# Performance work log

Hardware: AMD Instinct MI355X
Metric: run time of the kernel (lower is better)

Reference implementation:

```python
import jax, jax.numpy as jnp
import numpy as np

PIXEL_W = 1.0
EPS = 1e-8
BIG = 1e10


def extract_zero_crossings(s):
    """Vectorized marching-squares-style zero-crossing extraction.
    s: (H, W) SDF. Returns padded points (N, 2) float and validity mask (N,) bool,
    N = (H-1)*W + H*(W-1), in the same (vertical pairs first, then horizontal)
    order as the original python loops."""
    H, W = s.shape
    dt = s.dtype
    # vertical neighbor pairs (i, j) vs (i+1, j)
    v1, v2 = s[:-1, :], s[1:, :]
    ii = jnp.broadcast_to(jnp.arange(H - 1, dtype=dt)[:, None], (H - 1, W))
    jj = jnp.broadcast_to(jnp.arange(W, dtype=dt)[None, :], (H - 1, W))
    c1 = v1 == 0
    c2 = (~c1) & (v2 == 0)
    cx = (~c1) & (~c2) & (v1 * v2 < 0)
    alpha = jnp.abs(v1) / (jnp.abs(v1) + jnp.abs(v2) + EPS)
    row = jnp.where(c1, ii, jnp.where(c2, ii + 1.0, ii + alpha))
    pts_v = jnp.stack([row, jj], axis=-1).reshape(-1, 2)
    m_v = (c1 | c2 | cx).reshape(-1)
    # horizontal neighbor pairs (i, j) vs (i, j+1)
    h1, h2 = s[:, :-1], s[:, 1:]
    ii2 = jnp.broadcast_to(jnp.arange(H, dtype=dt)[:, None], (H, W - 1))
    jj2 = jnp.broadcast_to(jnp.arange(W - 1, dtype=dt)[None, :], (H, W - 1))
    d1 = h1 == 0
    d2 = (~d1) & (h2 == 0)
    dx = (~d1) & (~d2) & (h1 * h2 < 0)
    beta = jnp.abs(h1) / (jnp.abs(h1) + jnp.abs(h2) + EPS)
    col = jnp.where(d1, jj2, jnp.where(d2, jj2 + 1.0, jj2 + beta))
    pts_h = jnp.stack([ii2, col], axis=-1).reshape(-1, 2)
    m_h = (d1 | d2 | dx).reshape(-1)
    return jnp.concatenate([pts_v, pts_h], 0), jnp.concatenate([m_v, m_h], 0)


def pairwise_dist(p, g):
    # (Np, Ng) euclidean distances via the gram trick (avoids (Np,Ng,2) temp)
    d2 = jnp.sum(p * p, 1)[:, None] + jnp.sum(g * g, 1)[None, :] - 2.0 * (p @ g.T)
    return jnp.sqrt(jnp.maximum(d2, 0.0))


def masked_chamfer(pp, pm, gp, gm):
    # chamfer as in compute_chamfer_distance: -mean(min over gt) + mean(min over pred)
    d = pairwise_dist(pp, gp)
    d = jnp.where(pm[:, None] & gm[None, :], d, BIG)
    min_p = jnp.min(d, axis=1)
    min_g = jnp.min(d, axis=0)
    np_ = jnp.maximum(jnp.sum(pm), 1)
    ng_ = jnp.maximum(jnp.sum(gm), 1)
    return -jnp.sum(jnp.where(pm, min_p, 0.0)) / np_ + jnp.sum(jnp.where(gm, min_g, 0.0)) / ng_


def setup_inputs() -> dict:
    key = jax.random.key(0)
    k1, k2 = jax.random.split(key)
    B, H, W = 2, 80, 80
    return {
        "pred_logits": jax.random.normal(k1, (B, 1, H, W), dtype=jnp.float32),
        "gt_sdf": jax.random.normal(k2, (B, 1, H, W), dtype=jnp.float32),
    }


def reference(pred_logits, gt_sdf):
    pred = pred_logits[:, 0]  # (B, H, W)
    gt = gt_sdf[:, 0]
    pixel_loss = jnp.mean(jnp.abs(pred - gt))
    chamfers = []
    for b in range(pred.shape[0]):  # small fixed batch loop
        pp, pm = extract_zero_crossings(pred[b])
        gp, gm = extract_zero_crossings(gt[b])
        chamfers.append(masked_chamfer(pp, pm, gp, gm))
    loss = PIXEL_W * pixel_loss
    last_chamfer = jnp.mean(jnp.stack(chamfers))
    return loss, last_chamfer
```

## Files before the change

### kernel.cpp

```cpp
#include <hip/hip_runtime.h>

#define HH 80
#define WW 80
#define IMG (HH * WW)
#define NV ((HH - 1) * WW)
#define NPTS (NV + HH * (WW - 1))
#define NPIX (2 * IMG)
#define BIGF 1.0e10f
#define INVC 1.0e7f
#define EPSF 1e-8f
#define QSCALE 131072.0f

#define SETPAD 12800
#define SBLOCKS (SETPAD / 256)
#define EXBLOCKS (4 * SBLOCKS)
#define PXBLOCKS (NPIX / 256)
#define PREPB (EXBLOCKS + PXBLOCKS)

#define BLK 256
#define APT 8
#define ACHUNK (BLK * APT)
#define ABLOCKS ((NPTS + ACHUNK - 1) / ACHUNK)
#define NSLICE 64
#define MAXSLICE ((((NPTS + NSLICE - 1) / NSLICE) + 1) & ~1)
#define MAXP2 (MAXSLICE / 2)

#define CNT_STRIDE 32
#define PIX_OFF 512
#define TICKET_OFF 640
#define SUM_OFF 768
#define SCALAR_BYTES 1024

typedef float f32x2 __attribute__((ext_vector_type(2)));

__device__ __forceinline__ long long wave_reduce_ll(long long v) {
#pragma unroll
  for (int o = 32; o > 0; o >>= 1) {
    int2 p = *(int2*)&v;
    p.x = __shfl_down(p.x, o, 64);
    p.y = __shfl_down(p.y, o, 64);
    v += *(long long*)&p;
  }
  return v;
}

__global__ void k_zero(unsigned int* __restrict__ w) {
  w[threadIdx.x] = 0u;
}

__global__ void __launch_bounds__(256) k_prep(
    const float* __restrict__ pred, const float* __restrict__ gt,
    float2* __restrict__ pts, float* __restrict__ minarr,
    int* __restrict__ cnt, unsigned long long* __restrict__ pix_i) {
  __shared__ int wc[4], wo[4];
  __shared__ long long rl[4];
  int tid = threadIdx.x, lane = tid & 63, wid = tid >> 6;
  int gtid = blockIdx.x * 256 + tid;

  if (gtid < 4 * NPTS) minarr[gtid] = BIGF;

  if (blockIdx.x < EXBLOCKS) {
    int set = blockIdx.x / SBLOCKS;
    int idx = (blockIdx.x % SBLOCKS) * 256 + tid;
    const float* s = (set < 2 ? pred : gt) + (set & 1) * IMG;
    float r = 0.f, c = 0.f;
    bool valid = false;
    if (idx < NPTS) {
      if (idx < NV) {
        int i = idx / WW, j = idx - i * WW;
        float v1 = s[i * WW + j], v2 = s[(i + 1) * WW + j];
        c = (float)j;
        if (v1 == 0.f)      { r = (float)i;       valid = true; }
        else if (v2 == 0.f) { r = (float)i + 1.f; valid = true; }
        else {
          r = (float)i + fabsf(v1) / (fabsf(v1) + fabsf(v2) + EPSF);
          valid = (v1 * v2 < 0.f);
        }
      } else {
        int t = idx - NV;
        int i = t / (WW - 1), j = t - i * (WW - 1);
        float h1 = s[i * WW + j], h2 = s[i * WW + j + 1];
        r = (float)i;
        if (h1 == 0.f)      { c = (float)j;       valid = true; }
        else if (h2 == 0.f) { c = (float)j + 1.f; valid = true; }
        else {
          c = (float)j + fabsf(h1) / (fabsf(h1) + fabsf(h2) + EPSF);
          valid = (h1 * h2 < 0.f);
        }
      }
    }
    unsigned long long mask = __ballot(valid);
    int nw = __popcll(mask);
    if (lane == 0) wc[wid] = nw;
    __syncthreads();
    if (tid == 0) {
      int t0 = wc[0], t1 = wc[1], t2 = wc[2], t3 = wc[3];
      int tot = t0 + t1 + t2 + t3;
      int base = tot ? atomicAdd(&cnt[set * CNT_STRIDE], tot) : 0;
      wo[0] = base; wo[1] = base + t0; wo[2] = base + t0 + t1;
      wo[3] = base + t0 + t1 + t2;
    }
    __syncthreads();
    if (valid) {
      int lpos = __popcll(mask & ((1ull << lane) - 1ull));
      pts[set * NPTS + wo[wid] + lpos] = make_float2(r, c);
    }
  } else {
    int p = (blockIdx.x - EXBLOCKS) * 256 + tid;
    float d = fabsf(pred[p] - gt[p]);
    long long q = (long long)(d * QSCALE + 0.5f);
    q = wave_reduce_ll(q);
    if (lane == 0) rl[wid] = q;
    __syncthreads();
    if (tid == 0)
      atomicAdd(pix_i, (unsigned long long)(rl[0] + rl[1] + rl[2] + rl[3]));
  }
}

__global__ void __launch_bounds__(BLK) k_min(
    const float2* __restrict__ pts, float* __restrict__ minarr,
    const int* __restrict__ cnt) {
  int dir = blockIdx.z;
  int Aset = ((dir & 1) << 1) | (dir >> 1);
  int Bset = Aset ^ 2;
  int cntA = cnt[Aset * CNT_STRIDE], cntB = cnt[Bset * CNT_STRIDE];

  int abase0 = blockIdx.x * ACHUNK;
  if (abase0 >= cntA) return;
  int slicelen = (((cntB + NSLICE - 1) / NSLICE) + 1) & ~1;
  int b0 = blockIdx.y * slicelen;
  if (b0 >= cntB) return;
  int n = min(slicelen, cntB - b0);
  int sn = (n + 1) & ~1;

  __shared__ f32x2 qx_s[MAXP2], qy_s[MAXP2], q2_s[MAXP2];
  for (int i = threadIdx.x; i < sn; i += BLK) {
    float2 q = (i < n) ? pts[Bset * NPTS + b0 + i] : make_float2(INVC, INVC);
    ((float*)qx_s)[i] = q.x;
    ((float*)qy_s)[i] = q.y;
    ((float*)q2_s)[i] = fmaf(q.x, q.x, q.y * q.y);
  }
  __syncthreads();

  int abase = abase0 + threadIdx.x;
  f32x2 nxv[APT], nyv[APT];
  float p2v[APT], m[APT];
#pragma unroll
  for (int i = 0; i < APT; ++i) {
    int a = abase + i * BLK;
    float2 p = (a < cntA) ? pts[Aset * NPTS + a] : make_float2(0.f, 0.f);
    float nx = -2.f * p.x, ny = -2.f * p.y;
    nxv[i].x = nx; nxv[i].y = nx;
    nyv[i].x = ny; nyv[i].y = ny;
    p2v[i] = fmaf(p.x, p.x, p.y * p.y);
    m[i] = 3.0e38f;
  }

  int np2 = sn >> 1;
#pragma unroll 2
  for (int p = 0; p < np2; ++p) {
    f32x2 qx = qx_s[p], qy = qy_s[p], q2 = q2_s[p];
#pragma unroll
    for (int i = 0; i < APT; ++i) {
      f32x2 u = __builtin_elementwise_fma(
          nyv[i], qy, __builtin_elementwise_fma(nxv[i], qx, q2));
      m[i] = fminf(fminf(u.x, u.y), m[i]);
    }
  }

#pragma unroll
  for (int i = 0; i < APT; ++i) {
    int a = abase + i * BLK;
    if (a < cntA) {
      float d2 = fmaxf(m[i] + p2v[i], 0.f);
      unsigned int mine = __float_as_uint(d2);
      unsigned int* addr = (unsigned int*)&minarr[Aset * NPTS + a];
      unsigned int cur = __hip_atomic_load(addr, __ATOMIC_RELAXED,
                                           __HIP_MEMORY_SCOPE_AGENT);
      if (mine < cur) atomicMin(addr, mine);
    }
  }
}

__global__ void __launch_bounds__(256) k_fin(
    const float* __restrict__ minarr, const int* __restrict__ cnt,
    const unsigned long long* __restrict__ pix_i,
    unsigned long long* __restrict__ sum_i,
    unsigned int* __restrict__ ticket, float* __restrict__ out) {
  int set = blockIdx.x >> 2, q = blockIdx.x & 3;
  int tid = threadIdx.x, lane = tid & 63;
  int n = cnt[set * CNT_STRIDE];

  long long ls = 0;
  for (int i = q * 256 + tid; i < n; i += 1024) {
    float d = sqrtf(minarr[set * NPTS + i]);
    ls += (long long)(d * QSCALE + 0.5f);
  }
  ls = wave_reduce_ll(ls);
  if (lane == 0) atomicAdd(&sum_i[set], (unsigned long long)ls);
  __syncthreads();

  if (tid == 0) {
    __threadfence();
    unsigned int t = atomicAdd(ticket, 1u);
    if (t == 15u) {
      const float iq = 1.0f / QSCALE;
      float ss[4];
      for (int k = 0; k < 4; ++k)
        ss[k] = (float)((long long)atomicAdd(&sum_i[k], 0ull)) * iq;
      float n0 = fmaxf((float)cnt[0 * CNT_STRIDE], 1.f);
      float n1 = fmaxf((float)cnt[1 * CNT_STRIDE], 1.f);
      float n2 = fmaxf((float)cnt[2 * CNT_STRIDE], 1.f);
      float n3 = fmaxf((float)cnt[3 * CNT_STRIDE], 1.f);
      float ch0 = -ss[0] / n0 + ss[2] / n2;
      float ch1 = -ss[1] / n1 + ss[3] / n3;
      out[0] = (float)(long long)(*pix_i) * iq / (float)NPIX;
      out[1] = 0.5f * (ch0 + ch1);
    }
  }
}

extern "C" void kernel_launch(void* const* d_in, const int* in_sizes, int n_in,
                              void* d_out, int out_size, void* d_ws, size_t ws_size,
                              hipStream_t stream) {
  const float* pred = (const float*)d_in[0];
  const float* gt   = (const float*)d_in[1];
  float* out = (float*)d_out;

  int* cnt = (int*)d_ws;
  unsigned long long* pix_i = (unsigned long long*)((char*)d_ws + PIX_OFF);
  unsigned int* ticket = (unsigned int*)((char*)d_ws + TICKET_OFF);
  unsigned long long* sum_i = (unsigned long long*)((char*)d_ws + SUM_OFF);
  float2* pts   = (float2*)((char*)d_ws + SCALAR_BYTES);
  float* minarr = (float*)((char*)d_ws + SCALAR_BYTES + sizeof(float2) * 4 * NPTS);

  k_zero<<<1, 256, 0, stream>>>((unsigned int*)d_ws);
  k_prep<<<PREPB, 256, 0, stream>>>(pred, gt, pts, minarr, cnt, pix_i);
  k_min<<<dim3(ABLOCKS, NSLICE, 4), BLK, 0, stream>>>(pts, minarr, cnt);
  k_fin<<<16, 256, 0, stream>>>(minarr, cnt, pix_i, sum_i, ticket, out);
}
```

Baseline: 38.75 us.

## Replace global atomic compaction with per-segment counts and drop zeroing kernel

Zero-crossing points are now compacted per 256-wide segment with per-segment counts, not through a global atomic counter, so the separate zero-init kernel can be removed. The pixel loss goes into per-block partial sums that the final kernel reduces. The min kernel tiles over segment groups (8 A-segments by 2 B-segments), picks 4 or 8 points per thread from the count, and maps thread indices to segments with prefix offsets. This saves one launch and the atomic contention, at the cost of more index arithmetic and a fixed grid that may contain many empty or lightly loaded blocks.

Measured after the change: 43.57 us. 12.4% more time.

```diff
diff --git a/kernel.cpp b/kernel.cpp
--- a/kernel.cpp
+++ b/kernel.cpp
@@ -11,25 +11,18 @@
 #define EPSF 1e-8f
 #define QSCALE 131072.0f
 
-#define SETPAD 12800
-#define SBLOCKS (SETPAD / 256)
-#define EXBLOCKS (4 * SBLOCKS)
-#define PXBLOCKS (NPIX / 256)
+#define NSEG 50
+#define SEGPAD 64
+#define SETSLOTS (NSEG * 256)
+
+#define EXBLOCKS (4 * NSEG)
+#define PXBLOCKS 50
 #define PREPB (EXBLOCKS + PXBLOCKS)
 
 #define BLK 256
-#define APT 8
-#define ACHUNK (BLK * APT)
-#define ABLOCKS ((NPTS + ACHUNK - 1) / ACHUNK)
-#define NSLICE 64
-#define MAXSLICE ((((NPTS + NSLICE - 1) / NSLICE) + 1) & ~1)
-#define MAXP2 (MAXSLICE / 2)
-
-#define CNT_STRIDE 32
-#define PIX_OFF 512
-#define TICKET_OFF 640
-#define SUM_OFF 768
-#define SCALAR_BYTES 1024
+#define AGROUPS 7
+#define BSLICES 25
+#define MAXB 512
 
 typedef float f32x2 __attribute__((ext_vector_type(2)));
 
@@ -44,24 +37,22 @@
   return v;
 }
 
-__global__ void k_zero(unsigned int* __restrict__ w) {
-  w[threadIdx.x] = 0u;
-}
-
 __global__ void __launch_bounds__(256) k_prep(
     const float* __restrict__ pred, const float* __restrict__ gt,
     float2* __restrict__ pts, float* __restrict__ minarr,
-    int* __restrict__ cnt, unsigned long long* __restrict__ pix_i) {
+    int* __restrict__ scnt, unsigned int* __restrict__ zwords,
+    unsigned long long* __restrict__ pixpart) {
   __shared__ int wc[4], wo[4];
   __shared__ long long rl[4];
   int tid = threadIdx.x, lane = tid & 63, wid = tid >> 6;
-  int gtid = blockIdx.x * 256 + tid;
-
-  if (gtid < 4 * NPTS) minarr[gtid] = BIGF;
-
-  if (blockIdx.x < EXBLOCKS) {
-    int set = blockIdx.x / SBLOCKS;
-    int idx = (blockIdx.x % SBLOCKS) * 256 + tid;
+  int b = blockIdx.x;
+
+  if (b < EXBLOCKS) {
+    int set = b / NSEG, seg = b % NSEG;
+    minarr[set * SETSLOTS + seg * 256 + tid] = BIGF;
+    if (seg == 0 && tid >= NSEG && tid < SEGPAD) scnt[set * SEGPAD + tid] = 0;
+
+    int idx = seg * 256 + tid;
     const float* s = (set < 2 ? pred : gt) + (set & 1) * IMG;
     float r = 0.f, c = 0.f;
     bool valid = false;
@@ -95,65 +86,59 @@
     __syncthreads();
     if (tid == 0) {
       int t0 = wc[0], t1 = wc[1], t2 = wc[2], t3 = wc[3];
-      int tot = t0 + t1 + t2 + t3;
-      int base = tot ? atomicAdd(&cnt[set * CNT_STRIDE], tot) : 0;
-      wo[0] = base; wo[1] = base + t0; wo[2] = base + t0 + t1;
-      wo[3] = base + t0 + t1 + t2;
+      wo[0] = 0; wo[1] = t0; wo[2] = t0 + t1; wo[3] = t0 + t1 + t2;
+      scnt[set * SEGPAD + seg] = t0 + t1 + t2 + t3;
     }
     __syncthreads();
     if (valid) {
       int lpos = __popcll(mask & ((1ull << lane) - 1ull));
-      pts[set * NPTS + wo[wid] + lpos] = make_float2(r, c);
+      pts[(set * NSEG + seg) * 256 + wo[wid] + lpos] = make_float2(r, c);
     }
   } else {
-    int p = (blockIdx.x - EXBLOCKS) * 256 + tid;
+    int pb = b - EXBLOCKS;
+    if (pb == 0 && tid < 16) zwords[tid] = 0u;
+    int p = pb * 256 + tid;
     float d = fabsf(pred[p] - gt[p]);
     long long q = (long long)(d * QSCALE + 0.5f);
     q = wave_reduce_ll(q);
     if (lane == 0) rl[wid] = q;
     __syncthreads();
     if (tid == 0)
-      atomicAdd(pix_i, (unsigned long long)(rl[0] + rl[1] + rl[2] + rl[3]));
-  }
-}
-
-__global__ void __launch_bounds__(BLK) k_min(
+      pixpart[pb] = (unsigned long long)(rl[0] + rl[1] + rl[2] + rl[3]);
+  }
+}
+
+template <int APT>
+__device__ __forceinline__ void min_core(
+    int tid, int sn, int T,
+    int m1, int m2, int m3, int m4, int m5, int m6, int m7,
+    int segbase, int Aset,
     const float2* __restrict__ pts, float* __restrict__ minarr,
-    const int* __restrict__ cnt) {
-  int dir = blockIdx.z;
-  int Aset = ((dir & 1) << 1) | (dir >> 1);
-  int Bset = Aset ^ 2;
-  int cntA = cnt[Aset * CNT_STRIDE], cntB = cnt[Bset * CNT_STRIDE];
-
-  int abase0 = blockIdx.x * ACHUNK;
-  if (abase0 >= cntA) return;
-  int slicelen = (((cntB + NSLICE - 1) / NSLICE) + 1) & ~1;
-  int b0 = blockIdx.y * slicelen;
-  if (b0 >= cntB) return;
-  int n = min(slicelen, cntB - b0);
-  int sn = (n + 1) & ~1;
-
-  __shared__ f32x2 qx_s[MAXP2], qy_s[MAXP2], q2_s[MAXP2];
-  for (int i = threadIdx.x; i < sn; i += BLK) {
-    float2 q = (i < n) ? pts[Bset * NPTS + b0 + i] : make_float2(INVC, INVC);
-    ((float*)qx_s)[i] = q.x;
-    ((float*)qy_s)[i] = q.y;
-    ((float*)q2_s)[i] = fmaf(q.x, q.x, q.y * q.y);
-  }
-  __syncthreads();
-
-  int abase = abase0 + threadIdx.x;
+    const f32x2* qx_s, const f32x2* qy_s, const f32x2* q2_s) {
   f32x2 nxv[APT], nyv[APT];
   float p2v[APT], m[APT];
+  int slot[APT];
 #pragma unroll
   for (int i = 0; i < APT; ++i) {
-    int a = abase + i * BLK;
-    float2 p = (a < cntA) ? pts[Aset * NPTS + a] : make_float2(0.f, 0.f);
+    int d = tid + i * 256;
+    int k = 0, base = 0;
+    if (d >= m1) { k = 1; base = m1; }
+    if (d >= m2) { k = 2; base = m2; }
+    if (d >= m3) { k = 3; base = m3; }
+    if (d >= m4) { k = 4; base = m4; }
+    if (d >= m5) { k = 5; base = m5; }
+    if (d >= m6) { k = 6; base = m6; }
+    if (d >= m7) { k = 7; base = m7; }
+    bool valid = d < T;
+    int pos = d - base;
+    float2 p = valid ? pts[(Aset * NSEG + segbase + k) * 256 + pos]
+                     : make_float2(0.f, 0.f);
     float nx = -2.f * p.x, ny = -2.f * p.y;
     nxv[i].x = nx; nxv[i].y = nx;
     nyv[i].x = ny; nyv[i].y = ny;
     p2v[i] = fmaf(p.x, p.x, p.y * p.y);
     m[i] = 3.0e38f;
+    slot[i] = valid ? (Aset * SETSLOTS + (segbase + k) * 256 + pos) : -1;
   }
 
   int np2 = sn >> 1;
@@ -170,11 +155,10 @@
 
 #pragma unroll
   for (int i = 0; i < APT; ++i) {
-    int a = abase + i * BLK;
-    if (a < cntA) {
+    if (slot[i] >= 0) {
       float d2 = fmaxf(m[i] + p2v[i], 0.f);
       unsigned int mine = __float_as_uint(d2);
-      unsigned int* addr = (unsigned int*)&minarr[Aset * NPTS + a];
+      unsigned int* addr = (unsigned int*)&minarr[slot[i]];
       unsigned int cur = __hip_atomic_load(addr, __ATOMIC_RELAXED,
                                            __HIP_MEMORY_SCOPE_AGENT);
       if (mine < cur) atomicMin(addr, mine);
@@ -182,39 +166,103 @@
   }
 }
 
+__global__ void __launch_bounds__(BLK) k_min(
+    const float2* __restrict__ pts, float* __restrict__ minarr,
+    const int* __restrict__ scnt) {
+  __shared__ f32x2 qx_s[MAXB / 2 + 1], qy_s[MAXB / 2 + 1], q2_s[MAXB / 2 + 1];
+  int tid = threadIdx.x;
+  int dir = blockIdx.z;
+  int Aset = ((dir & 1) << 1) | (dir >> 1);
+  int Bset = Aset ^ 2;
+
+  int seg0 = blockIdx.y * 2;
+  int cb0 = scnt[Bset * SEGPAD + seg0];
+  int cb1 = scnt[Bset * SEGPAD + seg0 + 1];
+  const float2* bp0 = pts + (Bset * NSEG + seg0) * 256;
+  if (tid < cb0) {
+    float2 q = bp0[tid];
+    ((float*)qx_s)[tid] = q.x;
+    ((float*)qy_s)[tid] = q.y;
+    ((float*)q2_s)[tid] = fmaf(q.x, q.x, q.y * q.y);
+  }
+  if (tid < cb1) {
+    float2 q = bp0[256 + tid];
+    ((float*)qx_s)[cb0 + tid] = q.x;
+    ((float*)qy_s)[cb0 + tid] = q.y;
+    ((float*)q2_s)[cb0 + tid] = fmaf(q.x, q.x, q.y * q.y);
+  }
+  int nb = cb0 + cb1;
+  if ((nb & 1) && tid == 0) {
+    ((float*)qx_s)[nb] = INVC;
+    ((float*)qy_s)[nb] = INVC;
+    ((float*)q2_s)[nb] = fmaf(INVC, INVC, INVC * INVC);
+  }
+  int sn = (nb + 1) & ~1;
+  __syncthreads();
+
+  int segbase = blockIdx.x * 8;
+  const int* ac = scnt + Aset * SEGPAD + segbase;
+  int a0 = ac[0], a1 = ac[1], a2 = ac[2], a3 = ac[3];
+  int a4 = ac[4], a5 = ac[5], a6 = ac[6], a7 = ac[7];
+  int m1 = a0, m2 = m1 + a1, m3 = m2 + a2, m4 = m3 + a3;
+  int m5 = m4 + a4, m6 = m5 + a5, m7 = m6 + a6;
+  int T = m7 + a7;
+  if (T == 0 || nb == 0) return;
+
+  if (T <= 1024)
+    min_core<4>(tid, sn, T, m1, m2, m3, m4, m5, m6, m7, segbase, Aset,
+                pts, minarr, qx_s, qy_s, q2_s);
+  else
+    min_core<8>(tid, sn, T, m1, m2, m3, m4, m5, m6, m7, segbase, Aset,
+                pts, minarr, qx_s, qy_s, q2_s);
+}
+
 __global__ void __launch_bounds__(256) k_fin(
-    const float* __restrict__ minarr, const int* __restrict__ cnt,
-    const unsigned long long* __restrict__ pix_i,
-    unsigned long long* __restrict__ sum_i,
-    unsigned int* __restrict__ ticket, float* __restrict__ out) {
+    const float* __restrict__ minarr, const int* __restrict__ scnt,
+    const unsigned long long* __restrict__ pixpart,
+    unsigned int* __restrict__ ticket, unsigned int* __restrict__ cnttot,
+    unsigned long long* __restrict__ sum_i, float* __restrict__ out) {
+  __shared__ long long rls[4];
+  __shared__ long long pix_s;
   int set = blockIdx.x >> 2, q = blockIdx.x & 3;
-  int tid = threadIdx.x, lane = tid & 63;
-  int n = cnt[set * CNT_STRIDE];
+  int tid = threadIdx.x, lane = tid & 63, wid = tid >> 6;
+
+  if (wid == 0) {
+    long long pv = (lane < PXBLOCKS) ? (long long)pixpart[lane] : 0ll;
+    pv = wave_reduce_ll(pv);
+    if (lane == 0) pix_s = pv;
+  }
 
   long long ls = 0;
-  for (int i = q * 256 + tid; i < n; i += 1024) {
-    float d = sqrtf(minarr[set * NPTS + i]);
-    ls += (long long)(d * QSCALE + 0.5f);
+  int csum = 0;
+  for (int seg = q; seg < NSEG; seg += 4) {
+    int c = scnt[set * SEGPAD + seg];
+    csum += c;
+    if (tid < c) {
+      float d2 = minarr[set * SETSLOTS + seg * 256 + tid];
+      ls += (long long)(sqrtf(d2) * QSCALE + 0.5f);
+    }
   }
   ls = wave_reduce_ll(ls);
-  if (lane == 0) atomicAdd(&sum_i[set], (unsigned long long)ls);
+  if (lane == 0) rls[wid] = ls;
   __syncthreads();
 
   if (tid == 0) {
+    long long tot = rls[0] + rls[1] + rls[2] + rls[3];
+    atomicAdd(&sum_i[set], (unsigned long long)tot);
+    atomicAdd(&cnttot[set], (unsigned int)csum);
     __threadfence();
     unsigned int t = atomicAdd(ticket, 1u);
     if (t == 15u) {
       const float iq = 1.0f / QSCALE;
-      float ss[4];
-      for (int k = 0; k < 4; ++k)
+      float ss[4], nn[4];
+      for (int k = 0; k < 4; ++k) {
         ss[k] = (float)((long long)atomicAdd(&sum_i[k], 0ull)) * iq;
-      float n0 = fmaxf((float)cnt[0 * CNT_STRIDE], 1.f);
-      float n1 = fmaxf((float)cnt[1 * CNT_STRIDE], 1.f);
-      float n2 = fmaxf((float)cnt[2 * CNT_STRIDE], 1.f);
-      float n3 = fmaxf((float)cnt[3 * CNT_STRIDE], 1.f);
-      float ch0 = -ss[0] / n0 + ss[2] / n2;
-      float ch1 = -ss[1] / n1 + ss[3] / n3;
-      out[0] = (float)(long long)(*pix_i) * iq / (float)NPIX;
+        nn[k] = fmaxf((float)atomicAdd(&cnttot[k], 0u), 1.f);
+      }
+      float ch0 = -ss[0] / nn[0] + ss[2] / nn[2];
+      float ch1 = -ss[1] / nn[1] + ss[3] / nn[3];
+      out[0] = (float)pix_s * iq / (float)NPIX;
       out[1] = 0.5f * (ch0 + ch1);
     }
   }
@@ -227,15 +275,16 @@
   const float* gt   = (const float*)d_in[1];
   float* out = (float*)d_out;
 
-  int* cnt = (int*)d_ws;
-  unsigned long long* pix_i = (unsigned long long*)((char*)d_ws + PIX_OFF);
-  unsigned int* ticket = (unsigned int*)((char*)d_ws + TICKET_OFF);
-  unsigned long long* sum_i = (unsigned long long*)((char*)d_ws + SUM_OFF);
-  float2* pts   = (float2*)((char*)d_ws + SCALAR_BYTES);
-  float* minarr = (float*)((char*)d_ws + SCALAR_BYTES + sizeof(float2) * 4 * NPTS);
-
-  k_zero<<<1, 256, 0, stream>>>((unsigned int*)d_ws);
-  k_prep<<<PREPB, 256, 0, stream>>>(pred, gt, pts, minarr, cnt, pix_i);
-  k_min<<<dim3(ABLOCKS, NSLICE, 4), BLK, 0, stream>>>(pts, minarr, cnt);
-  k_fin<<<16, 256, 0, stream>>>(minarr, cnt, pix_i, sum_i, ticket, out);
-}
+  int* scnt = (int*)d_ws;
+  unsigned int* zwords = (unsigned int*)((char*)d_ws + 1024);
+  unsigned int* ticket = zwords;
+  unsigned int* cnttot = zwords + 1;
+  unsigned long long* sum_i = (unsigned long long*)((char*)d_ws + 1056);
+  unsigned long long* pixpart = (unsigned long long*)((char*)d_ws + 1152);
+  float2* pts = (float2*)((char*)d_ws + 2048);
+  float* minarr = (float*)((char*)d_ws + 2048 + sizeof(float2) * 4 * SETSLOTS);
+
+  k_prep<<<PREPB, 256, 0, stream>>>(pred, gt, pts, minarr, scnt, zwords, pixpart);
+  k_min<<<dim3(AGROUPS, BSLICES, 4), BLK, 0, stream>>>(pts, minarr, scnt);
+  k_fin<<<16, 256, 0, stream>>>(minarr, scnt, pixpart, ticket, cnttot, sum_i, out);
+}
```
